# Optimization experiments

Measured on AMD Instinct MI355X. Metric: run time of the kernel, lower is better.

Reference implementation:

```python
import jax, jax.numpy as jnp
import numpy as np

BATCH, SEQ, DIM, NUM_CODES = 8, 2048, 1024, 8192

def setup_inputs() -> dict:
    key = jax.random.key(0)
    kx, kc = jax.random.split(key)
    x = jax.random.normal(kx, (BATCH, SEQ, DIM), dtype=jnp.float32)
    # nn.Embedding default init: N(0, 1)
    codebook = jax.random.normal(kc, (NUM_CODES, DIM), dtype=jnp.float32)
    return {"x": x, "codebook": codebook}

def reference(x, codebook):
    # tau=0 path of CodebookLayer.forward (SnapFunction.forward):
    # similarity logits [B, S, num_codes], nearest-code argmax, gather.
    logits = jnp.einsum('bsd,cd->bsc', x, codebook)
    codebook_ids = jnp.argmax(logits, axis=-1)            # [B, S] int
    output = jnp.take(codebook, codebook_ids, axis=0)     # [B, S, D]
    return output
```

## Files before the change

### kernel.cpp

```cpp
#include <hip/hip_runtime.h>
#include <stdint.h>


#define T_TOKENS 16384
#define N_CODES  8192
#define DIM      1024
#define BM 128
#define BN 128
#define BK 64
#define NBLK (N_CODES / BM)
#define KITERS (DIM / BK)
#define EPS 13.0f
#define MAXCAND 48

typedef int   int8v  __attribute__((ext_vector_type(8)));
typedef int   int4v  __attribute__((ext_vector_type(4)));
typedef float f32x16 __attribute__((ext_vector_type(16)));

#define GLD16(gp, lp) \
  __builtin_amdgcn_global_load_lds((__attribute__((address_space(1))) void*)(gp), \
                                   (__attribute__((address_space(3))) void*)(lp), 16, 0, 0)

__device__ inline uint32_t umax(uint32_t a, uint32_t b) { return a > b ? a : b; }
__device__ inline uint32_t umin(uint32_t a, uint32_t b) { return a < b ? a : b; }
__device__ inline uint32_t umed3(uint32_t a, uint32_t b, uint32_t c) {
  return umax(umin(a, b), umin(umax(a, b), c));
}

__device__ inline uint32_t f32_key(float v) {
  int32_t b = (int32_t)__float_as_uint(v);
  return (uint32_t)(b ^ ((b >> 31) | (int32_t)0x80000000));
}
__device__ inline float key_f32(uint32_t u) {
  uint32_t b = (u & 0x80000000u) ? (u & 0x7FFFFFFFu) : ~u;
  return __uint_as_float(b);
}

__global__ __launch_bounds__(256) void vq_prep(const float* __restrict__ x,
                                               const float* __restrict__ cbm,
                                               uint8_t* __restrict__ xq,
                                               uint8_t* __restrict__ cq) {
  size_t b = blockIdx.x;
  const float* src; uint8_t* dst;
  if (b < 16384) { src = x;  dst = xq; }
  else           { b -= 16384; src = cbm; dst = cq; }
  const size_t i = b * 256 + threadIdx.x;
  const float4 v = ((const float4*)src)[i];
  uint32_t r = __builtin_amdgcn_cvt_pk_fp8_f32(v.x, v.y, 0, false);
  r = __builtin_amdgcn_cvt_pk_fp8_f32(v.z, v.w, (int)r, true);
  ((uint32_t*)dst)[i] = r;
}

__global__ __launch_bounds__(256) void vq_gemm_top3(
    const uint8_t* __restrict__ cq,
    const uint8_t* __restrict__ xq,
    uint32_t* __restrict__ pk)
{
  __shared__ uint8_t smem[2][2 * BM * BK];

  const int t    = threadIdx.x;
  const int wave = t >> 6;
  const int lane = t & 63;
  const int col  = lane & 31;
  const int hi   = lane >> 5;
  const int cb0  = blockIdx.y * BM;
  const int tb0  = blockIdx.x * BN;
  const int wm   = (wave >> 1) * 64;
  const int wn   = (wave & 1) * 64;

  const int c0 = t, c1 = t + 256;
  const int r0 = c0 >> 2, k0 = ((c0 & 3) ^ ((r0 >> 1) & 3)) * 16;
  const int r1 = c1 >> 2, k1 = ((c1 & 3) ^ ((r1 >> 1) & 3)) * 16;

  const uint8_t* pa0 = cq + (size_t)(cb0 + r0) * DIM + k0;
  const uint8_t* pa1 = cq + (size_t)(cb0 + r1) * DIM + k1;
  const uint8_t* pb0 = xq + (size_t)(tb0 + r0) * DIM + k0;
  const uint8_t* pb1 = xq + (size_t)(tb0 + r1) * DIM + k1;

  f32x16 acc[2][2];
#pragma unroll
  for (int i = 0; i < 2; ++i)
#pragma unroll
    for (int j = 0; j < 2; ++j)
#pragma unroll
      for (int r = 0; r < 16; ++r) acc[i][j][r] = 0.f;

  {
    uint8_t* As = smem[0];
    uint8_t* Bs = smem[0] + BM * BK;
    GLD16(pa0, As + c0 * 16); GLD16(pa1, As + c1 * 16);
    GLD16(pb0, Bs + c0 * 16); GLD16(pb1, Bs + c1 * 16);
    pa0 += BK; pa1 += BK; pb0 += BK; pb1 += BK;
  }
  __syncthreads();

  for (int kt = 0; kt < KITERS; ++kt) {
    if (kt != KITERS - 1) {
      uint8_t* As = smem[(kt + 1) & 1];
      uint8_t* Bs = smem[(kt + 1) & 1] + BM * BK;
      GLD16(pa0, As + c0 * 16); GLD16(pa1, As + c1 * 16);
      GLD16(pb0, Bs + c0 * 16); GLD16(pb1, Bs + c1 * 16);
      pa0 += BK; pa1 += BK; pb0 += BK; pb1 += BK;
    }

    const uint8_t* As = smem[kt & 1];
    const uint8_t* Bs = smem[kt & 1] + BM * BK;
    int8v a[2], b[2];
    const int j0 = hi * 2;
#pragma unroll
    for (int i = 0; i < 2; ++i) {
      const int ra = wm + i * 32 + col;
      const int pa = (ra >> 1) & 3;
      const int4v alo = *(const int4v*)(As + (ra * 4 + (j0 ^ pa)) * 16);
      const int4v ahi = *(const int4v*)(As + (ra * 4 + ((j0 + 1) ^ pa)) * 16);
      a[i] = (int8v){alo[0], alo[1], alo[2], alo[3], ahi[0], ahi[1], ahi[2], ahi[3]};
      const int rb = wn + i * 32 + col;
      const int pb = (rb >> 1) & 3;
      const int4v blo = *(const int4v*)(Bs + (rb * 4 + (j0 ^ pb)) * 16);
      const int4v bhi = *(const int4v*)(Bs + (rb * 4 + ((j0 + 1) ^ pb)) * 16);
      b[i] = (int8v){blo[0], blo[1], blo[2], blo[3], bhi[0], bhi[1], bhi[2], bhi[3]};
    }
#pragma unroll
    for (int i = 0; i < 2; ++i)
#pragma unroll
      for (int j = 0; j < 2; ++j)
        acc[i][j] = __builtin_amdgcn_mfma_scale_f32_32x32x64_f8f6f4(
            a[i], b[j], acc[i][j], 0, 0, 0, 0x7F7F7F7F, 0, 0x7F7F7F7F);
    __syncthreads();
  }

  uint32_t* cand = (uint32_t*)smem;
  const int invb = 127 - wm - 4 * hi;
#pragma unroll
  for (int j = 0; j < 2; ++j) {
    uint32_t K1 = 0, K2 = 0, K3 = 0;
#pragma unroll
    for (int i = 0; i < 2; ++i) {
#pragma unroll
      for (int rg = 0; rg < 16; ++rg) {
        const int rowoff = (rg & 3) + 8 * (rg >> 2);
        const uint32_t key = (f32_key(acc[i][j][rg]) & 0xFFFFFF80u)
                           | (uint32_t)(invb - i * 32 - rowoff);
        const uint32_t t3 = umed3(key, K2, K3);
        const uint32_t t2 = umed3(key, K1, K2);
        K1 = umax(key, K1); K2 = t2; K3 = t3;
      }
    }
    const uint32_t o1 = __shfl_xor(K1, 32, 64);
    const uint32_t o2 = __shfl_xor(K2, 32, 64);
    const uint32_t o3 = __shfl_xor(K3, 32, 64);
    const uint32_t m1 = umin(K1, o1), M2 = umax(K2, o2);
    const uint32_t m2 = umin(K2, o2), M3 = umax(K3, o3);
    K1 = umax(K1, o1);
    const uint32_t nk2 = umax(m1, M2);
    K3 = umax(umax(m2, umin(m1, M2)), M3);
    K2 = nk2;
    if (hi == 0) {
      uint32_t* c = &cand[((wn + j * 32 + col) * 2 + (wave >> 1)) * 3];
      c[0] = K1; c[1] = K2; c[2] = K3;
    }
  }
  __syncthreads();
  if (t < BN) {
    const uint32_t a1 = cand[(t * 2 + 0) * 3 + 0], a2 = cand[(t * 2 + 0) * 3 + 1],
                   a3 = cand[(t * 2 + 0) * 3 + 2];
    const uint32_t b1 = cand[(t * 2 + 1) * 3 + 0], b2 = cand[(t * 2 + 1) * 3 + 1],
                   b3 = cand[(t * 2 + 1) * 3 + 2];
    const uint32_t m1 = umin(a1, b1), M2 = umax(a2, b2);
    const uint32_t m2 = umin(a2, b2), M3 = umax(a3, b3);
    uint32_t* dst = pk + ((size_t)(tb0 + t) * NBLK + blockIdx.y) * 3;
    dst[0] = umax(a1, b1);
    dst[1] = umax(m1, M2);
    dst[2] = umax(umax(m2, umin(m1, M2)), M3);
  }
}

__global__ __launch_bounds__(256) void vq_reduce_gather(
    const uint32_t* __restrict__ pk, const float* __restrict__ x,
    const float* __restrict__ cb, float* __restrict__ out)
{
  __shared__ float xs[DIM];
  __shared__ uint32_t wmax[4];
  __shared__ int scand[MAXCAND];
  __shared__ int scnt;
  __shared__ double sdot[MAXCAND];
  __shared__ int sbesti;

  const int tkn = blockIdx.x, t = threadIdx.x, lane = t & 63, wv = t >> 6;
  ((float4*)xs)[t] = ((const float4*)(x + (size_t)tkn * DIM))[t];
  const uint32_t key = (t < 3 * NBLK) ? pk[(size_t)tkn * (3 * NBLK) + t] : 0u;
  uint32_t m = key;
#pragma unroll
  for (int d = 1; d < 64; d <<= 1) m = umax(m, __shfl_xor(m, d, 64));
  if (t == 0) scnt = 0;
  if (lane == 0) wmax[wv] = m;
  __syncthreads();
  const float Mv = key_f32(umax(umax(wmax[0], wmax[1]), umax(wmax[2], wmax[3])));
  if (t < 3 * NBLK && key_f32(key) >= Mv - EPS) {
    const int p = atomicAdd(&scnt, 1);
    if (p < MAXCAND) scand[p] = (t / 3) * BM + 127 - (int)(key & 127u);
  }
  __syncthreads();
  const int cnt = scnt < MAXCAND ? scnt : MAXCAND;

  if (cnt > 1) {
    for (int k = wv; k < cnt; k += 4) {
      const int c = scand[k];
      const float* cr = cb + (size_t)c * DIM;
      double s = 0.0;
#pragma unroll
      for (int q = 0; q < 4; ++q) {
        const float4 xv = ((const float4*)xs)[lane + 64 * q];
        const float4 cv = ((const float4*)cr)[lane + 64 * q];
        s += (double)xv.x * cv.x + (double)xv.y * cv.y
           + (double)xv.z * cv.z + (double)xv.w * cv.w;
      }
#pragma unroll
      for (int d = 1; d < 64; d <<= 1) s += __shfl_xor(s, d, 64);
      if (lane == 0) sdot[k] = s;
    }
    __syncthreads();
    if (t == 0) {
      double best = -1e300; int bi = N_CODES;
      for (int k = 0; k < cnt; ++k) {
        const int c = scand[k];
        if (sdot[k] > best || (sdot[k] == best && c < bi)) { best = sdot[k]; bi = c; }
      }
      sbesti = bi;
    }
  } else {
    if (t == 0) sbesti = scand[0];
  }
  __syncthreads();
  const int code = sbesti;
  ((float4*)(out + (size_t)tkn * DIM))[t] = ((const float4*)(cb + (size_t)code * DIM))[t];
}

__global__ __launch_bounds__(256) void vq_naive(const float* __restrict__ x,
                                                const float* __restrict__ cb,
                                                float* __restrict__ out) {
  __shared__ float xs[DIM];
  __shared__ float bv[256];
  __shared__ int   bix[256];
  const int tkn = blockIdx.x;
  const int t = threadIdx.x;
  for (int d = t; d < DIM; d += 256) xs[d] = x[(size_t)tkn * DIM + d];
  __syncthreads();
  float best = -1e30f; int bi = N_CODES;
  for (int c = t; c < N_CODES; c += 256) {
    const float* cr = cb + (size_t)c * DIM;
    float s = 0.f;
    for (int d = 0; d < DIM; ++d) s += xs[d] * cr[d];
    if (s > best || (s == best && c < bi)) { best = s; bi = c; }
  }
  bv[t] = best; bix[t] = bi;
  __syncthreads();
  for (int off = 128; off > 0; off >>= 1) {
    if (t < off) {
      if (bv[t + off] > bv[t] || (bv[t + off] == bv[t] && bix[t + off] < bix[t])) {
        bv[t] = bv[t + off]; bix[t] = bix[t + off];
      }
    }
    __syncthreads();
  }
  const int code = bix[0];
  for (int d = t; d < DIM; d += 256)
    out[(size_t)tkn * DIM + d] = cb[(size_t)code * DIM + d];
}

extern "C" void kernel_launch(void* const* d_in, const int* in_sizes, int n_in,
                              void* d_out, int out_size, void* d_ws, size_t ws_size,
                              hipStream_t stream) {
  const float* x  = (const float*)d_in[0];
  const float* cb = (const float*)d_in[1];
  float* out = (float*)d_out;

  const size_t MB = 1024 * 1024;
  const size_t need = 24 * MB + (size_t)T_TOKENS * NBLK * 3 * 4;
  if (ws_size >= need) {
    uint8_t*  xq = (uint8_t*)d_ws;
    uint8_t*  cq = xq + 16 * MB;
    uint32_t* pk = (uint32_t*)(cq + 8 * MB);

    vq_prep<<<dim3(24576), 256, 0, stream>>>(x, cb, xq, cq);
    vq_gemm_top3<<<dim3(T_TOKENS / BN, N_CODES / BM), 256, 0, stream>>>(cq, xq, pk);
    vq_reduce_gather<<<dim3(T_TOKENS), 256, 0, stream>>>(pk, x, cb, out);
  } else {
    vq_naive<<<dim3(T_TOKENS), 256, 0, stream>>>(x, cb, out);
  }
}
```

Measured before the change: 346.6 us.

## Enlarge FP8 GEMM tiles to 256x256 with 4-stage LDS pipeline

The FP8 MFMA GEMM moves from 128x128 tiles with 4 waves to 256x256 tiles with 8 waves, and from double to quad buffering in LDS. Loads are issued two stages ahead with explicit vmcnt waits and barriers, MFMAs run at raised priority, and block indices are remapped with a swizzle for L2 locality. Larger tiles raise arithmetic intensity and halve the number of per-code-block candidates written to the reduce kernel. In exchange, the top-3 key keeps one fewer mantissa bit, and the code now uses 128KB of LDS and more registers, which lowers occupancy.

New measurement: 352.9 us. No clear change (+1.8%).

```diff
diff --git a/kernel.cpp b/kernel.cpp
--- a/kernel.cpp
+++ b/kernel.cpp
@@ -5,8 +5,8 @@
 #define T_TOKENS 16384
 #define N_CODES  8192
 #define DIM      1024
-#define BM 128
-#define BN 128
+#define BM 256
+#define BN 256
 #define BK 64
 #define NBLK (N_CODES / BM)
 #define KITERS (DIM / BK)
@@ -51,96 +51,131 @@
   ((uint32_t*)dst)[i] = r;
 }
 
-__global__ __launch_bounds__(256) void vq_gemm_top3(
+#define MFMA8(A_, B_, C_) \
+  __builtin_amdgcn_mfma_scale_f32_32x32x64_f8f6f4((A_), (B_), (C_), 0, 0, 0, \
+                                                  0x7F7F7F7F, 0, 0x7F7F7F7F)
+
+__global__ __launch_bounds__(512) void vq_gemm_top3(
     const uint8_t* __restrict__ cq,
     const uint8_t* __restrict__ xq,
     uint32_t* __restrict__ pk)
 {
-  __shared__ uint8_t smem[2][2 * BM * BK];
+  __shared__ uint8_t smem[4 * 32768];
 
   const int t    = threadIdx.x;
   const int wave = t >> 6;
   const int lane = t & 63;
   const int col  = lane & 31;
   const int hi   = lane >> 5;
-  const int cb0  = blockIdx.y * BM;
-  const int tb0  = blockIdx.x * BN;
-  const int wm   = (wave >> 1) * 64;
-  const int wn   = (wave & 1) * 64;
-
-  const int c0 = t, c1 = t + 256;
-  const int r0 = c0 >> 2, k0 = ((c0 & 3) ^ ((r0 >> 1) & 3)) * 16;
-  const int r1 = c1 >> 2, k1 = ((c1 & 3) ^ ((r1 >> 1) & 3)) * 16;
-
-  const uint8_t* pa0 = cq + (size_t)(cb0 + r0) * DIM + k0;
-  const uint8_t* pa1 = cq + (size_t)(cb0 + r1) * DIM + k1;
-  const uint8_t* pb0 = xq + (size_t)(tb0 + r0) * DIM + k0;
-  const uint8_t* pb1 = xq + (size_t)(tb0 + r1) * DIM + k1;
-
-  f32x16 acc[2][2];
-#pragma unroll
-  for (int i = 0; i < 2; ++i)
+  const int wm   = wave >> 2;
+  const int wn2  = (wave & 3) * 64;
+
+  const int f   = blockIdx.x;
+  const int swz = (f & 7) * 256 + (f >> 3);
+  const int cyi = swz >> 6;
+  const int tb0 = (swz & 63) * BN;
+  const int cb0 = cyi * BM;
+
+  const int r0 = t >> 2;
+  const int js = ((t & 3) ^ ((r0 >> 1) & 3)) * 16;
+  const uint8_t* sA0 = cq + (size_t)(cb0 + r0) * DIM + js;
+  const uint8_t* sA1 = cq + (size_t)(cb0 + r0 + 128) * DIM + js;
+  const uint8_t* sB0 = xq + (size_t)(tb0 + r0) * DIM + js;
+  const uint8_t* sB1 = xq + (size_t)(tb0 + r0 + 128) * DIM + js;
+
+#define STAGE(bi, ti) do {                                     \
+    uint8_t* Ad_ = smem + ((bi) << 15);                        \
+    const int ko_ = (ti) * BK;                                 \
+    GLD16(sA0 + ko_, Ad_ + t * 16);                            \
+    GLD16(sA1 + ko_, Ad_ + (t + 512) * 16);                    \
+    GLD16(sB0 + ko_, Ad_ + 16384 + t * 16);                    \
+    GLD16(sB1 + ko_, Ad_ + 16384 + (t + 512) * 16);            \
+  } while (0)
+
+  const int j0 = hi * 2;
+  int aoff[4][2], boff[2][2];
+#pragma unroll
+  for (int mi = 0; mi < 4; ++mi) {
+    const int ra = wm * 128 + mi * 32 + col;
+    const int pa = (ra >> 1) & 3;
+    aoff[mi][0] = ra * 64 + (j0 ^ pa) * 16;
+    aoff[mi][1] = ra * 64 + ((j0 + 1) ^ pa) * 16;
+  }
+#pragma unroll
+  for (int jj = 0; jj < 2; ++jj) {
+    const int rb = wn2 + jj * 32 + col;
+    const int pb = (rb >> 1) & 3;
+    boff[jj][0] = 16384 + rb * 64 + (j0 ^ pb) * 16;
+    boff[jj][1] = 16384 + rb * 64 + ((j0 + 1) ^ pb) * 16;
+  }
+
+#define READ8(dst_, o0_, o1_) do {                                         \
+    const int4v lo_ = *(const int4v*)(cur + (o0_));                        \
+    const int4v hq_ = *(const int4v*)(cur + (o1_));                        \
+    dst_ = (int8v){lo_[0], lo_[1], lo_[2], lo_[3],                         \
+                   hq_[0], hq_[1], hq_[2], hq_[3]};                        \
+  } while (0)
+
+  f32x16 acc[4][2];
+#pragma unroll
+  for (int i = 0; i < 4; ++i)
 #pragma unroll
     for (int j = 0; j < 2; ++j)
 #pragma unroll
       for (int r = 0; r < 16; ++r) acc[i][j][r] = 0.f;
 
-  {
-    uint8_t* As = smem[0];
-    uint8_t* Bs = smem[0] + BM * BK;
-    GLD16(pa0, As + c0 * 16); GLD16(pa1, As + c1 * 16);
-    GLD16(pb0, Bs + c0 * 16); GLD16(pb1, Bs + c1 * 16);
-    pa0 += BK; pa1 += BK; pb0 += BK; pb1 += BK;
-  }
-  __syncthreads();
-
+  STAGE(0, 0);
+  STAGE(1, 1);
+
+#pragma unroll 4
   for (int kt = 0; kt < KITERS; ++kt) {
-    if (kt != KITERS - 1) {
-      uint8_t* As = smem[(kt + 1) & 1];
-      uint8_t* Bs = smem[(kt + 1) & 1] + BM * BK;
-      GLD16(pa0, As + c0 * 16); GLD16(pa1, As + c1 * 16);
-      GLD16(pb0, Bs + c0 * 16); GLD16(pb1, Bs + c1 * 16);
-      pa0 += BK; pa1 += BK; pb0 += BK; pb1 += BK;
-    }
-
-    const uint8_t* As = smem[kt & 1];
-    const uint8_t* Bs = smem[kt & 1] + BM * BK;
-    int8v a[2], b[2];
-    const int j0 = hi * 2;
-#pragma unroll
-    for (int i = 0; i < 2; ++i) {
-      const int ra = wm + i * 32 + col;
-      const int pa = (ra >> 1) & 3;
-      const int4v alo = *(const int4v*)(As + (ra * 4 + (j0 ^ pa)) * 16);
-      const int4v ahi = *(const int4v*)(As + (ra * 4 + ((j0 + 1) ^ pa)) * 16);
-      a[i] = (int8v){alo[0], alo[1], alo[2], alo[3], ahi[0], ahi[1], ahi[2], ahi[3]};
-      const int rb = wn + i * 32 + col;
-      const int pb = (rb >> 1) & 3;
-      const int4v blo = *(const int4v*)(Bs + (rb * 4 + (j0 ^ pb)) * 16);
-      const int4v bhi = *(const int4v*)(Bs + (rb * 4 + ((j0 + 1) ^ pb)) * 16);
-      b[i] = (int8v){blo[0], blo[1], blo[2], blo[3], bhi[0], bhi[1], bhi[2], bhi[3]};
-    }
-#pragma unroll
-    for (int i = 0; i < 2; ++i)
-#pragma unroll
-      for (int j = 0; j < 2; ++j)
-        acc[i][j] = __builtin_amdgcn_mfma_scale_f32_32x32x64_f8f6f4(
-            a[i], b[j], acc[i][j], 0, 0, 0, 0x7F7F7F7F, 0, 0x7F7F7F7F);
-    __syncthreads();
-  }
-
-  uint32_t* cand = (uint32_t*)smem;
-  const int invb = 127 - wm - 4 * hi;
+    asm volatile("s_waitcnt vmcnt(4)" ::: "memory");
+    __builtin_amdgcn_s_barrier();
+    __builtin_amdgcn_sched_barrier(0);
+
+    const uint8_t* cur = smem + ((kt & 3) << 15);
+    STAGE((kt + 2) & 3, (kt + 2) & 15);
+
+    int8v a[4], b0, b1;
+#pragma unroll
+    for (int mi = 0; mi < 4; ++mi) READ8(a[mi], aoff[mi][0], aoff[mi][1]);
+    READ8(b0, boff[0][0], boff[0][1]);
+    __builtin_amdgcn_s_barrier();
+    asm volatile("s_waitcnt lgkmcnt(0)" ::: "memory");
+    __builtin_amdgcn_sched_barrier(0);
+    __builtin_amdgcn_s_setprio(1);
+    acc[0][0] = MFMA8(a[0], b0, acc[0][0]);
+    acc[1][0] = MFMA8(a[1], b0, acc[1][0]);
+    acc[2][0] = MFMA8(a[2], b0, acc[2][0]);
+    acc[3][0] = MFMA8(a[3], b0, acc[3][0]);
+    __builtin_amdgcn_s_setprio(0);
+    __builtin_amdgcn_s_barrier();
+
+    READ8(b1, boff[1][0], boff[1][1]);
+    __builtin_amdgcn_s_barrier();
+    asm volatile("s_waitcnt lgkmcnt(0)" ::: "memory");
+    __builtin_amdgcn_sched_barrier(0);
+    __builtin_amdgcn_s_setprio(1);
+    acc[0][1] = MFMA8(a[0], b1, acc[0][1]);
+    acc[1][1] = MFMA8(a[1], b1, acc[1][1]);
+    acc[2][1] = MFMA8(a[2], b1, acc[2][1]);
+    acc[3][1] = MFMA8(a[3], b1, acc[3][1]);
+    __builtin_amdgcn_s_setprio(0);
+  }
+  __syncthreads();
+
+  uint32_t* cand = (uint32_t*)(smem + 2 * 32768);
+  const int invb = 255 - wm * 128 - 4 * hi;
 #pragma unroll
   for (int j = 0; j < 2; ++j) {
     uint32_t K1 = 0, K2 = 0, K3 = 0;
 #pragma unroll
-    for (int i = 0; i < 2; ++i) {
+    for (int mi = 0; mi < 4; ++mi) {
 #pragma unroll
       for (int rg = 0; rg < 16; ++rg) {
         const int rowoff = (rg & 3) + 8 * (rg >> 2);
-        const uint32_t key = (f32_key(acc[i][j][rg]) & 0xFFFFFF80u)
-                           | (uint32_t)(invb - i * 32 - rowoff);
+        const uint32_t key = (f32_key(acc[mi][j][rg]) & 0xFFFFFF00u)
+                           | (uint32_t)(invb - mi * 32 - rowoff);
         const uint32_t t3 = umed3(key, K2, K3);
         const uint32_t t2 = umed3(key, K1, K2);
         K1 = umax(key, K1); K2 = t2; K3 = t3;
@@ -156,7 +191,7 @@
     K3 = umax(umax(m2, umin(m1, M2)), M3);
     K2 = nk2;
     if (hi == 0) {
-      uint32_t* c = &cand[((wn + j * 32 + col) * 2 + (wave >> 1)) * 3];
+      uint32_t* c = &cand[((wn2 + j * 32 + col) * 2 + wm) * 3];
       c[0] = K1; c[1] = K2; c[2] = K3;
     }
   }
@@ -164,15 +199,17 @@
   if (t < BN) {
     const uint32_t a1 = cand[(t * 2 + 0) * 3 + 0], a2 = cand[(t * 2 + 0) * 3 + 1],
                    a3 = cand[(t * 2 + 0) * 3 + 2];
-    const uint32_t b1 = cand[(t * 2 + 1) * 3 + 0], b2 = cand[(t * 2 + 1) * 3 + 1],
+    const uint32_t b1k = cand[(t * 2 + 1) * 3 + 0], b2 = cand[(t * 2 + 1) * 3 + 1],
                    b3 = cand[(t * 2 + 1) * 3 + 2];
-    const uint32_t m1 = umin(a1, b1), M2 = umax(a2, b2);
+    const uint32_t m1 = umin(a1, b1k), M2 = umax(a2, b2);
     const uint32_t m2 = umin(a2, b2), M3 = umax(a3, b3);
-    uint32_t* dst = pk + ((size_t)(tb0 + t) * NBLK + blockIdx.y) * 3;
-    dst[0] = umax(a1, b1);
+    uint32_t* dst = pk + ((size_t)(tb0 + t) * NBLK + cyi) * 3;
+    dst[0] = umax(a1, b1k);
     dst[1] = umax(m1, M2);
     dst[2] = umax(umax(m2, umin(m1, M2)), M3);
   }
+#undef STAGE
+#undef READ8
 }
 
 __global__ __launch_bounds__(256) void vq_reduce_gather(
@@ -198,7 +235,7 @@
   const float Mv = key_f32(umax(umax(wmax[0], wmax[1]), umax(wmax[2], wmax[3])));
   if (t < 3 * NBLK && key_f32(key) >= Mv - EPS) {
     const int p = atomicAdd(&scnt, 1);
-    if (p < MAXCAND) scand[p] = (t / 3) * BM + 127 - (int)(key & 127u);
+    if (p < MAXCAND) scand[p] = (t / 3) * BM + 255 - (int)(key & 255u);
   }
   __syncthreads();
   const int cnt = scnt < MAXCAND ? scnt : MAXCAND;
@@ -283,7 +320,7 @@
     uint32_t* pk = (uint32_t*)(cq + 8 * MB);
 
     vq_prep<<<dim3(24576), 256, 0, stream>>>(x, cb, xq, cq);
-    vq_gemm_top3<<<dim3(T_TOKENS / BN, N_CODES / BM), 256, 0, stream>>>(cq, xq, pk);
+    vq_gemm_top3<<<dim3((T_TOKENS / BN) * (N_CODES / BM)), 512, 0, stream>>>(cq, xq, pk);
     vq_reduce_gather<<<dim3(T_TOKENS), 256, 0, stream>>>(pk, x, cb, out);
   } else {
     vq_naive<<<dim3(T_TOKENS), 256, 0, stream>>>(x, cb, out);
```
